# Kernel optimization log

Measured on AMD Instinct MI355X. Metric: run time of the kernel, lower is better.

The kernel has to match this reference:

```python
import jax, jax.numpy as jnp
import numpy as np

WIN = (2, 7, 7)
SHIFT = (1, 3, 3)
HEADS = 4
DIM = 128
MLP_HID = 512
N = WIN[0] * WIN[1] * WIN[2]  # 98
EPS = 1e-5


def _rel_pos_index():
    d = np.arange(WIN[0]); h = np.arange(WIN[1]); w = np.arange(WIN[2])
    coords = np.stack(np.meshgrid(d, h, w, indexing='ij'))  # (3, Wd, Wh, Ww)
    flat = coords.reshape(3, -1)  # (3, N)
    rel = flat[:, :, None] - flat[:, None, :]  # (3, N, N)
    rel = rel.transpose(1, 2, 0).astype(np.int64)  # (N, N, 3)
    rel[..., 0] += WIN[0] - 1
    rel[..., 1] += WIN[1] - 1
    rel[..., 2] += WIN[2] - 1
    rel[..., 0] *= (2 * WIN[1] - 1) * (2 * WIN[2] - 1)
    rel[..., 1] *= (2 * WIN[2] - 1)
    return rel.sum(-1)  # (N, N)


def setup_inputs() -> dict:
    key = jax.random.key(0)
    ks = jax.random.split(key, 8)
    B, D, H, W, C = 4, 8, 56, 56, DIM
    tbl_size = (2 * WIN[0] - 1) * (2 * WIN[1] - 1) * (2 * WIN[2] - 1)  # 507
    s = 0.02
    return {
        'x': jax.random.normal(ks[0], (B, D, H, W, C), jnp.float32),
        'rel_idx': jnp.asarray(_rel_pos_index(), jnp.int32),
        'rpb_table': s * jax.random.normal(ks[1], (tbl_size, HEADS), jnp.float32),
        'qkv_w': s * jax.random.normal(ks[2], (C, 3 * C), jnp.float32),
        'qkv_b': jnp.zeros((3 * C,), jnp.float32),
        'proj_w': s * jax.random.normal(ks[3], (C, C), jnp.float32),
        'proj_b': jnp.zeros((C,), jnp.float32),
        'ln1_g': jnp.ones((C,), jnp.float32),
        'ln1_b': jnp.zeros((C,), jnp.float32),
        'ln2_g': jnp.ones((C,), jnp.float32),
        'ln2_b': jnp.zeros((C,), jnp.float32),
        'mlp_w1': s * jax.random.normal(ks[4], (C, MLP_HID), jnp.float32),
        'mlp_b1': jnp.zeros((MLP_HID,), jnp.float32),
        'mlp_w2': s * jax.random.normal(ks[5], (MLP_HID, C), jnp.float32),
        'mlp_b2': jnp.zeros((C,), jnp.float32),
    }


def _layernorm(x, g, b):
    mu = jnp.mean(x, -1, keepdims=True)
    var = jnp.var(x, -1, keepdims=True)
    return (x - mu) * jax.lax.rsqrt(var + EPS) * g + b


def _window_partition(x):
    B, Dp, Hp, Wp, C = x.shape
    x = x.reshape(B, Dp // WIN[0], WIN[0], Hp // WIN[1], WIN[1], Wp // WIN[2], WIN[2], C)
    x = x.transpose(0, 1, 3, 5, 2, 4, 6, 7)
    return x.reshape(-1, N, C)


def _window_reverse(win, B, Dp, Hp, Wp):
    C = win.shape[-1]
    x = win.reshape(B, Dp // WIN[0], Hp // WIN[1], Wp // WIN[2], WIN[0], WIN[1], WIN[2], C)
    x = x.transpose(0, 1, 4, 2, 5, 3, 6, 7)
    return x.reshape(B, Dp, Hp, Wp, C)


def _block(x, rel_idx, rpb_table, qkv_w, qkv_b, proj_w, proj_b,
           ln1_g, ln1_b, ln2_g, ln2_b, mlp_w1, mlp_b1, mlp_w2, mlp_b2):
    B, D, H, W, C = x.shape
    shortcut = x
    x = _layernorm(x, ln1_g, ln1_b)
    pad_d = (-D) % WIN[0]; pad_h = (-H) % WIN[1]; pad_w = (-W) % WIN[2]
    x = jnp.pad(x, ((0, 0), (0, pad_d), (0, pad_h), (0, pad_w), (0, 0)))
    _, Dp, Hp, Wp, _ = x.shape
    x = jnp.roll(x, (-SHIFT[0], -SHIFT[1], -SHIFT[2]), axis=(1, 2, 3))
    xw = _window_partition(x)  # (B_, N, C)
    B_ = xw.shape[0]
    hd = C // HEADS
    qkv = (xw @ qkv_w + qkv_b).reshape(B_, N, 3, HEADS, hd).transpose(2, 0, 3, 1, 4)
    q, k, v = qkv[0], qkv[1], qkv[2]  # (B_, h, N, hd)
    q = q * (hd ** -0.5)
    attn = jnp.einsum('bhnd,bhmd->bhnm', q, k)
    bias = rpb_table[rel_idx.reshape(-1)].reshape(N, N, HEADS).transpose(2, 0, 1)
    attn = attn + bias[None]
    # NOTE: the original module calls attn with mask=None even when shifted.
    attn = jax.nn.softmax(attn, axis=-1)
    out = jnp.einsum('bhnm,bhmd->bhnd', attn, v).transpose(0, 2, 1, 3).reshape(B_, N, C)
    out = out @ proj_w + proj_b
    x = _window_reverse(out, B, Dp, Hp, Wp)
    x = jnp.roll(x, (SHIFT[0], SHIFT[1], SHIFT[2]), axis=(1, 2, 3))
    x = x[:, :D, :H, :W, :]
    x = shortcut + x
    h1 = _layernorm(x, ln2_g, ln2_b)
    h1 = jax.nn.gelu(h1 @ mlp_w1 + mlp_b1, approximate=False)
    return x + (h1 @ mlp_w2 + mlp_b2)


def reference(x, rel_idx, rpb_table, qkv_w, qkv_b, proj_w, proj_b,
              ln1_g, ln1_b, ln2_g, ln2_b, mlp_w1, mlp_b1, mlp_w2, mlp_b2):
    return _block(x, rel_idx, rpb_table, qkv_w, qkv_b, proj_w, proj_b,
                  ln1_g, ln1_b, ln2_g, ln2_b, mlp_w1, mlp_b1, mlp_w2, mlp_b2)
```

## Files before the change

### kernel.cpp

```cpp
#include <hip/hip_runtime.h>
#include <hip/hip_bf16.h>
#include <cstdint>

#define NWIN   1024
#define NTOK   98
#define BIAS_N 9604

typedef __attribute__((ext_vector_type(8))) short bf16x8;
typedef __attribute__((ext_vector_type(4))) float f32x4;

__device__ __forceinline__ float b2f(unsigned short u) {
  union { uint32_t i; float f; } v; v.i = ((uint32_t)u) << 16; return v.f;
}
__device__ __forceinline__ float b2f_lo(uint32_t u) {
  union { uint32_t i; float f; } v; v.i = u << 16; return v.f;
}
__device__ __forceinline__ float b2f_hi(uint32_t u) {
  union { uint32_t i; float f; } v; v.i = u & 0xffff0000u; return v.f;
}
__device__ __forceinline__ unsigned short f2b(float f) {
  union { float f; uint32_t i; } v; v.f = f;
  uint32_t r = v.i + 0x7fffu + ((v.i >> 16) & 1u);
  return (unsigned short)(r >> 16);
}
__device__ __forceinline__ float ldf(const void* p, size_t i, int f32) {
  return f32 ? ((const float*)p)[i] : b2f(((const unsigned short*)p)[i]);
}
__device__ __forceinline__ void stf(void* p, size_t i, int f32, float v) {
  if (f32) ((float*)p)[i] = v;
  else     ((unsigned short*)p)[i] = f2b(v);
}
__device__ __forceinline__ float2 ldf2(const void* p, size_t i, int f32) {
  if (f32) { const float* q = (const float*)p + i; return make_float2(q[0], q[1]); }
  uint32_t u = *(const uint32_t*)((const unsigned short*)p + i);
  return make_float2(b2f_lo(u), b2f_hi(u));
}

#define QG_OFF   0
#define KG_OFF   25690112
#define VGT_OFF  51380224
#define ZPAD_OFF 80740352
#define BIAS_OFF 80748544
#define WQ_OFF   80902208
#define WP_OFF   81000512
#define W1_OFF   81033280
#define W2_OFF   81164352
#define PAR_OFF  81295424
#define FLAG_OFF 81302080
#define P_LN1G 0
#define P_LN1B 128
#define P_LN2G 256
#define P_LN2B 384
#define P_QKVB 512
#define P_PROJB 896
#define P_B1  1024
#define P_B2  1536

__global__ __launch_bounds__(256) void detect_kernel(const uint32_t* __restrict__ xw,
                                                     int* __restrict__ flag) {
  __shared__ int cnt;
  if (threadIdx.x == 0) cnt = 0;
  __syncthreads();
  uint32_t w = xw[threadIdx.x];
  int e = (w >> 23) & 0xFF;
  if (e >= 112 && e <= 134) atomicAdd(&cnt, 1);
  __syncthreads();
  if (threadIdx.x == 0) *flag = (cnt >= 128) ? 1 : 0;
}

__global__ __launch_bounds__(256) void prep_kernel(
    const void* __restrict__ qkvw, const void* __restrict__ projw,
    const void* __restrict__ w1, const void* __restrict__ w2,
    const void* __restrict__ ln1g, const void* __restrict__ ln1b,
    const void* __restrict__ ln2g, const void* __restrict__ ln2b,
    const void* __restrict__ qkvb, const void* __restrict__ projb,
    const void* __restrict__ b1, const void* __restrict__ b2,
    const int* __restrict__ flag,
    unsigned short* __restrict__ wq_t, unsigned short* __restrict__ wp_t,
    unsigned short* __restrict__ w1_t, unsigned short* __restrict__ w2_t,
    float* __restrict__ par, unsigned short* __restrict__ zpad) {
  const int f32 = *flag;
  int idx = blockIdx.x * 256 + threadIdx.x;
  if (idx < 49152) {
    int n = idx >> 7, k = idx & 127;
    wq_t[idx] = f2b(ldf(qkvw, (size_t)k * 384 + n, f32));
  } else if ((idx -= 49152) < 16384) {
    int n = idx >> 7, k = idx & 127;
    wp_t[idx] = f2b(ldf(projw, (size_t)k * 128 + n, f32));
  } else if ((idx -= 16384) < 65536) {
    int n = idx >> 7, k = idx & 127;
    w1_t[idx] = f2b(ldf(w1, (size_t)k * 512 + n, f32));
  } else if ((idx -= 65536) < 65536) {
    int n = idx >> 9, k = idx & 511;
    w2_t[idx] = f2b(ldf(w2, (size_t)k * 128 + n, f32));
  } else if ((idx -= 65536) < 1664) {
    float v;
    if      (idx < 128)  v = ldf(ln1g, idx, f32);
    else if (idx < 256)  v = ldf(ln1b, idx - 128, f32);
    else if (idx < 384)  v = ldf(ln2g, idx - 256, f32);
    else if (idx < 512)  v = ldf(ln2b, idx - 384, f32);
    else if (idx < 896)  v = ldf(qkvb, idx - 512, f32);
    else if (idx < 1024) v = ldf(projb, idx - 896, f32);
    else if (idx < 1536) v = ldf(b1, idx - 1024, f32);
    else                 v = ldf(b2, idx - 1536, f32);
    par[idx] = v;
  } else if ((idx -= 1664) < 4096) {
    zpad[idx] = 0;
  }
}

__global__ __launch_bounds__(256) void bias_kernel(const int* __restrict__ rel_idx,
                                                   const void* __restrict__ tbl,
                                                   const int* __restrict__ flag,
                                                   float* __restrict__ bias) {
  const int f32 = *flag;
  int i = blockIdx.x * 256 + threadIdx.x;
  if (i >= 4 * BIAS_N) return;
  int h = i / BIAS_N, ij = i % BIAS_N;
  bias[i] = ldf(tbl, (size_t)rel_idx[ij] * 4 + h, f32);
}

__global__ __launch_bounds__(256) void qkv_win_kernel(
    const void* __restrict__ x, const int* __restrict__ flag,
    const unsigned short* __restrict__ wq_t, const float* __restrict__ par,
    unsigned short* __restrict__ qg, unsigned short* __restrict__ kg,
    unsigned short* __restrict__ vgt) {
  __shared__ unsigned short lnx[112 * 136];
  const int f32 = *flag;
  const int tid = threadIdx.x, wave = tid >> 6, lane = tid & 63;
  const int quad = lane >> 4, lcol = lane & 15;
  const int win = blockIdx.x;
  const int bb = win >> 8, r = win & 255;
  const int wd = r >> 6, r2 = r & 63, wh = r2 >> 3, ww = r2 & 7;

  for (int t = wave; t < NTOK; t += 4) {
    int td = t / 49, r3 = t % 49, th = r3 / 7, tw = r3 % 7;
    int sd = (wd * 2 + td + 1) & 7;
    int sh = (wh * 7 + th + 3) % 56;
    int sw = (ww * 7 + tw + 3) % 56;
    size_t src = ((((size_t)bb * 8 + sd) * 56 + sh) * 56 + sw) * 128;
    int c0 = lane * 2;
    float2 f = ldf2(x, src + c0, f32);
    float s = f.x + f.y, ss = f.x * f.x + f.y * f.y;
#pragma unroll
    for (int off = 32; off >= 1; off >>= 1) { s += __shfl_xor(s, off); ss += __shfl_xor(ss, off); }
    float mu = s * (1.0f / 128.0f);
    float var = ss * (1.0f / 128.0f) - mu * mu;
    float rs = rsqrtf(var + 1e-5f);
    float y0 = (f.x - mu) * rs * par[P_LN1G + c0] + par[P_LN1B + c0];
    float y1 = (f.y - mu) * rs * par[P_LN1G + c0 + 1] + par[P_LN1B + c0 + 1];
    *(uint32_t*)(lnx + t * 136 + c0) = (uint32_t)f2b(y0) | ((uint32_t)f2b(y1) << 16);
  }
  for (int i = tid; i < 14 * 68; i += 256) {
    int rr = i / 68, c = i % 68;
    *(uint32_t*)(lnx + (98 + rr) * 136 + c * 2) = 0u;
  }
  __syncthreads();

  for (int p = 0; p < 6; ++p) {
    const int n = p * 64 + wave * 16 + lcol;
    bf16x8 bfr[4];
#pragma unroll
    for (int ks = 0; ks < 4; ++ks)
      bfr[ks] = *(const bf16x8*)(wq_t + (size_t)n * 128 + ks * 32 + quad * 8);
    const int region = n >> 7, cc = n & 127, head = cc >> 5, d = cc & 31;
    const float bc = par[P_QKVB + n];
    if (region < 2) {
      unsigned short* dst = (region == 0 ? qg : kg) +
                            (((size_t)win * 4 + head) * NTOK) * 32 + d;
      const float scale = region == 0 ? 0.17677669529663687f : 1.0f;
      for (int mt = 0; mt < 7; ++mt) {
        f32x4 acc = (f32x4){0.f, 0.f, 0.f, 0.f};
#pragma unroll
        for (int ks = 0; ks < 4; ++ks) {
          bf16x8 a = *(const bf16x8*)(lnx + (mt * 16 + lcol) * 136 + ks * 32 + quad * 8);
          acc = __builtin_amdgcn_mfma_f32_16x16x32_bf16(a, bfr[ks], acc, 0, 0, 0);
        }
#pragma unroll
        for (int rr = 0; rr < 4; ++rr) {
          int m = mt * 16 + quad * 4 + rr;
          if (m < NTOK) dst[m * 32] = f2b((acc[rr] + bc) * scale);
        }
      }
    } else {
      unsigned short* dstv = vgt + (((size_t)win * 4 + head) * 32 + d) * 112;
      for (int mt = 0; mt < 7; ++mt) {
        f32x4 acc = (f32x4){0.f, 0.f, 0.f, 0.f};
#pragma unroll
        for (int ks = 0; ks < 4; ++ks) {
          bf16x8 a = *(const bf16x8*)(lnx + (mt * 16 + lcol) * 136 + ks * 32 + quad * 8);
          acc = __builtin_amdgcn_mfma_f32_16x16x32_bf16(a, bfr[ks], acc, 0, 0, 0);
        }
        ushort4 w;
        int m0 = mt * 16 + quad * 4;
        w.x = (m0 + 0 < NTOK) ? f2b(acc[0] + bc) : (unsigned short)0;
        w.y = (m0 + 1 < NTOK) ? f2b(acc[1] + bc) : (unsigned short)0;
        w.z = (m0 + 2 < NTOK) ? f2b(acc[2] + bc) : (unsigned short)0;
        w.w = (m0 + 3 < NTOK) ? f2b(acc[3] + bc) : (unsigned short)0;
        *(ushort4*)(dstv + m0) = w;
      }
    }
  }
}

__global__ __launch_bounds__(256, 4) void attn_fused_kernel(
    const unsigned short* __restrict__ qg, const unsigned short* __restrict__ kg,
    const unsigned short* __restrict__ vgt, const float* __restrict__ bias,
    const unsigned short* __restrict__ wp_t, const float* __restrict__ par,
    const void* __restrict__ x, const int* __restrict__ flag,
    void* __restrict__ out) {
  __shared__ __align__(16) unsigned short smem[15232];
  const int f32 = *flag;
  const int tid = threadIdx.x, wave = tid >> 6, lane = tid & 63;
  const int quad = lane >> 4, lcol = lane & 15;
  const int win = blockIdx.x, h = wave;
  const size_t hb = (((size_t)win * 4 + h) * NTOK) * 32;
  const unsigned short* vbase = vgt + (((size_t)win * 4 + h) * 32) * 112;

  unsigned short* plh = smem + h * (16 * 132);

  for (int idx = lane; idx < 16 * 16; idx += 64) {
    int rr = idx >> 4, c = 112 + (idx & 15);
    plh[rr * 132 + c] = 0;
  }

  bf16x8 aq[7], bk[7];
#pragma unroll
  for (int t = 0; t < 7; ++t) {
    int row = min(t * 16 + lcol, NTOK - 1);
    aq[t] = *(const bf16x8*)(qg + hb + (size_t)row * 32 + quad * 8);
    bk[t] = *(const bf16x8*)(kg + hb + (size_t)row * 32 + quad * 8);
  }

  const float* bh = bias + h * BIAS_N;
  f32x4 o[7][2];
  for (int mt = 0; mt < 7; ++mt) {
    f32x4 s[7];
#pragma unroll
    for (int nt = 0; nt < 7; ++nt)
      s[nt] = __builtin_amdgcn_mfma_f32_16x16x32_bf16(aq[mt], bk[nt],
                                                      (f32x4){0.f, 0.f, 0.f, 0.f}, 0, 0, 0);
    const int ib = mt * 16 + quad * 4;
#pragma unroll
    for (int nt = 0; nt < 7; ++nt) {
      int j = nt * 16 + lcol;
      bool jv = j < NTOK;
#pragma unroll
      for (int r = 0; r < 4; ++r) {
        int ic = min(ib + r, NTOK - 1);
        s[nt][r] = jv ? (s[nt][r] + bh[ic * NTOK + j]) : -3.0e38f;
      }
    }
    float mx[4], sum[4], inv[4];
#pragma unroll
    for (int r = 0; r < 4; ++r) {
      float m = s[0][r];
#pragma unroll
      for (int nt = 1; nt < 7; ++nt) m = fmaxf(m, s[nt][r]);
      mx[r] = m;
    }
#pragma unroll
    for (int off = 1; off < 16; off <<= 1)
#pragma unroll
      for (int r = 0; r < 4; ++r) mx[r] = fmaxf(mx[r], __shfl_xor(mx[r], off));
#pragma unroll
    for (int r = 0; r < 4; ++r) sum[r] = 0.f;
#pragma unroll
    for (int nt = 0; nt < 7; ++nt)
#pragma unroll
      for (int r = 0; r < 4; ++r) {
        float e = __expf(s[nt][r] - mx[r]);
        s[nt][r] = e; sum[r] += e;
      }
#pragma unroll
    for (int off = 1; off < 16; off <<= 1)
#pragma unroll
      for (int r = 0; r < 4; ++r) sum[r] += __shfl_xor(sum[r], off);
#pragma unroll
    for (int r = 0; r < 4; ++r) inv[r] = 1.0f / sum[r];
#pragma unroll
    for (int nt = 0; nt < 7; ++nt)
#pragma unroll
      for (int r = 0; r < 4; ++r)
        plh[(quad * 4 + r) * 132 + nt * 16 + lcol] = f2b(s[nt][r] * inv[r]);
#pragma unroll
    for (int n2 = 0; n2 < 2; ++n2) {
      f32x4 acc = (f32x4){0.f, 0.f, 0.f, 0.f};
#pragma unroll
      for (int kp = 0; kp < 4; ++kp) {
        bf16x8 a = *(const bf16x8*)(plh + lcol * 132 + kp * 32 + quad * 8);
        bf16x8 b = *(const bf16x8*)(vbase + (size_t)(n2 * 16 + lcol) * 112 +
                                    kp * 32 + quad * 8);
        acc = __builtin_amdgcn_mfma_f32_16x16x32_bf16(a, b, acc, 0, 0, 0);
      }
      o[mt][n2] = acc;
    }
  }
  __syncthreads();

  unsigned short* olds = smem;
#pragma unroll
  for (int mt = 0; mt < 7; ++mt)
#pragma unroll
    for (int n2 = 0; n2 < 2; ++n2)
#pragma unroll
      for (int r = 0; r < 4; ++r)
        olds[(mt * 16 + quad * 4 + r) * 136 + h * 32 + n2 * 16 + lcol] = f2b(o[mt][n2][r]);
  __syncthreads();

  f32x4 pr[2][7];
  for (int t2 = 0; t2 < 2; ++t2) {
    const int n = (h * 2 + t2) * 16 + lcol;
    bf16x8 bw[4];
#pragma unroll
    for (int kp = 0; kp < 4; ++kp)
      bw[kp] = *(const bf16x8*)(wp_t + (size_t)n * 128 + kp * 32 + quad * 8);
    for (int mt = 0; mt < 7; ++mt) {
      f32x4 acc = (f32x4){0.f, 0.f, 0.f, 0.f};
#pragma unroll
      for (int kp = 0; kp < 4; ++kp) {
        bf16x8 a = *(const bf16x8*)(olds + (mt * 16 + lcol) * 136 + kp * 32 + quad * 8);
        acc = __builtin_amdgcn_mfma_f32_16x16x32_bf16(a, bw[kp], acc, 0, 0, 0);
      }
      pr[t2][mt] = acc;
    }
  }
  __syncthreads();

  const int bb = win >> 8, rW = win & 255;
  const int wd = rW >> 6, r2 = rW & 63, wh = r2 >> 3, ww = r2 & 7;
  float* pout = (float*)smem;
  for (int pass = 0; pass < 2; ++pass) {
    const int mlo = pass * 56;
    for (int t2 = 0; t2 < 2; ++t2) {
      const int n = (h * 2 + t2) * 16 + lcol;
      const float bc = par[P_PROJB + n];
#pragma unroll
      for (int mt = 0; mt < 7; ++mt)
#pragma unroll
        for (int r = 0; r < 4; ++r) {
          int m = mt * 16 + quad * 4 + r;
          if (m >= mlo && m < mlo + 56 && m < NTOK)
            pout[(m - mlo) * 132 + n] = pr[t2][mt][r] + bc;
        }
    }
    __syncthreads();
    const int c = (tid & 31) * 4;
    for (int i = tid >> 5; i < 56; i += 8) {
      int m = mlo + i;
      if (m >= NTOK) break;
      int td = m / 49, r3 = m % 49, th = r3 / 7, tw = r3 % 7;
      int sd = (wd * 2 + td + 1) & 7;
      int sh = (wh * 7 + th + 3) % 56;
      int sw = (ww * 7 + tw + 3) % 56;
      size_t base = ((((size_t)bb * 8 + sd) * 56 + sh) * 56 + sw) * 128 + c;
      float4 p = *(const float4*)(pout + i * 132 + c);
      if (f32) {
        const float4 xr = *(const float4*)((const float*)x + base);
        float4 ov = make_float4(p.x + xr.x, p.y + xr.y, p.z + xr.z, p.w + xr.w);
        *(float4*)((float*)out + base) = ov;
      } else {
        const ushort4 xr = *(const ushort4*)((const unsigned short*)x + base);
        ushort4 ov;
        ov.x = f2b(p.x + b2f(xr.x)); ov.y = f2b(p.y + b2f(xr.y));
        ov.z = f2b(p.z + b2f(xr.z)); ov.w = f2b(p.w + b2f(xr.w));
        *(ushort4*)((unsigned short*)out + base) = ov;
      }
    }
    if (pass == 0) __syncthreads();
  }
}

__global__ __launch_bounds__(256) void mlp_kernel(
    const unsigned short* __restrict__ w1_t, const unsigned short* __restrict__ w2_t,
    const float* __restrict__ par, const int* __restrict__ flag,
    void* __restrict__ out) {
  __shared__ __align__(16) unsigned short lnt[32 * 136];
  __shared__ __align__(16) unsigned short hbuf[32 * 264];
  const int f32 = *flag;
  const int tid = threadIdx.x, wave = tid >> 6, lane = tid & 63;
  const int quad = lane >> 4, lcol = lane & 15;
  const int m0 = blockIdx.x * 32;

  for (int t = wave; t < 32; t += 4) {
    int c0 = lane * 2;
    float2 f = ldf2(out, (size_t)(m0 + t) * 128 + c0, f32);
    float s = f.x + f.y, ss = f.x * f.x + f.y * f.y;
#pragma unroll
    for (int off = 32; off >= 1; off >>= 1) { s += __shfl_xor(s, off); ss += __shfl_xor(ss, off); }
    float mu = s * (1.0f / 128.0f);
    float var = ss * (1.0f / 128.0f) - mu * mu;
    float rs = rsqrtf(var + 1e-5f);
    float y0 = (f.x - mu) * rs * par[P_LN2G + c0] + par[P_LN2B + c0];
    float y1 = (f.y - mu) * rs * par[P_LN2G + c0 + 1] + par[P_LN2B + c0 + 1];
    *(uint32_t*)(lnt + t * 136 + c0) = (uint32_t)f2b(y0) | ((uint32_t)f2b(y1) << 16);
  }
  __syncthreads();

  f32x4 acc2[2][2];
#pragma unroll
  for (int a = 0; a < 2; ++a)
#pragma unroll
    for (int b = 0; b < 2; ++b) acc2[a][b] = (f32x4){0.f, 0.f, 0.f, 0.f};

  for (int g = 0; g < 2; ++g) {
    for (int p = 0; p < 4; ++p) {
      const int nl = p * 64 + wave * 16 + lcol;
      const int n = g * 256 + nl;
      bf16x8 bfr[4];
#pragma unroll
      for (int ks = 0; ks < 4; ++ks)
        bfr[ks] = *(const bf16x8*)(w1_t + (size_t)n * 128 + ks * 32 + quad * 8);
      const float bc = par[P_B1 + n];
#pragma unroll
      for (int mt = 0; mt < 2; ++mt) {
        f32x4 acc = (f32x4){0.f, 0.f, 0.f, 0.f};
#pragma unroll
        for (int ks = 0; ks < 4; ++ks) {
          bf16x8 a = *(const bf16x8*)(lnt + (mt * 16 + lcol) * 136 + ks * 32 + quad * 8);
          acc = __builtin_amdgcn_mfma_f32_16x16x32_bf16(a, bfr[ks], acc, 0, 0, 0);
        }
#pragma unroll
        for (int rr = 0; rr < 4; ++rr) {
          int m = mt * 16 + quad * 4 + rr;
          float v = acc[rr] + bc;
          v = 0.5f * v * (1.0f + erff(v * 0.70710678118654752f));
          hbuf[m * 264 + nl] = f2b(v);
        }
      }
    }
    __syncthreads();

#pragma unroll
    for (int np = 0; np < 2; ++np) {
      const int n = np * 64 + wave * 16 + lcol;
      for (int kp = 0; kp < 2; ++kp) {
        bf16x8 bfr[4];
#pragma unroll
        for (int ks = 0; ks < 4; ++ks)
          bfr[ks] = *(const bf16x8*)(w2_t + (size_t)n * 512 + g * 256 + kp * 128 +
                                     ks * 32 + quad * 8);
#pragma unroll
        for (int mt = 0; mt < 2; ++mt) {
#pragma unroll
          for (int ks = 0; ks < 4; ++ks) {
            bf16x8 a = *(const bf16x8*)(hbuf + (mt * 16 + lcol) * 264 + kp * 128 +
                                        ks * 32 + quad * 8);
            acc2[np][mt] = __builtin_amdgcn_mfma_f32_16x16x32_bf16(a, bfr[ks], acc2[np][mt], 0, 0, 0);
          }
        }
      }
    }
    __syncthreads();
  }

  float* pout = (float*)hbuf;
#pragma unroll
  for (int np = 0; np < 2; ++np) {
    const int n = np * 64 + wave * 16 + lcol;
    const float bc = par[P_B2 + n];
#pragma unroll
    for (int mt = 0; mt < 2; ++mt)
#pragma unroll
      for (int rr = 0; rr < 4; ++rr)
        pout[(mt * 16 + quad * 4 + rr) * 132 + n] = acc2[np][mt][rr] + bc;
  }
  __syncthreads();

  for (int i = tid; i < 1024; i += 256) {
    int t = i >> 5, c = (i & 31) * 4;
    size_t base = (size_t)(m0 + t) * 128 + c;
    float4 p = *(const float4*)(pout + t * 132 + c);
    if (f32) {
      const float4 xr = *(const float4*)((const float*)out + base);
      float4 ov = make_float4(p.x + xr.x, p.y + xr.y, p.z + xr.z, p.w + xr.w);
      *(float4*)((float*)out + base) = ov;
    } else {
      const ushort4 xr = *(const ushort4*)((const unsigned short*)out + base);
      ushort4 ov;
      ov.x = f2b(p.x + b2f(xr.x)); ov.y = f2b(p.y + b2f(xr.y));
      ov.z = f2b(p.z + b2f(xr.z)); ov.w = f2b(p.w + b2f(xr.w));
      *(ushort4*)((unsigned short*)out + base) = ov;
    }
  }
}

extern "C" void kernel_launch(void* const* d_in, const int* in_sizes, int n_in,
                              void* d_out, int out_size, void* d_ws, size_t ws_size,
                              hipStream_t stream) {
  const void* x      = d_in[0];
  const int*  rel    = (const int*)d_in[1];
  const void* rpb    = d_in[2];
  const void* qkv_w  = d_in[3];
  const void* qkv_b  = d_in[4];
  const void* proj_w = d_in[5];
  const void* proj_b = d_in[6];
  const void* ln1_g  = d_in[7];
  const void* ln1_b  = d_in[8];
  const void* ln2_g  = d_in[9];
  const void* ln2_b  = d_in[10];
  const void* w1     = d_in[11];
  const void* b1     = d_in[12];
  const void* w2     = d_in[13];
  const void* b2     = d_in[14];

  char* ws = (char*)d_ws;
  unsigned short* qg   = (unsigned short*)(ws + QG_OFF);
  unsigned short* kg   = (unsigned short*)(ws + KG_OFF);
  unsigned short* vgt  = (unsigned short*)(ws + VGT_OFF);
  unsigned short* zpad = (unsigned short*)(ws + ZPAD_OFF);
  float*          bias = (float*)(ws + BIAS_OFF);
  unsigned short* wq_t = (unsigned short*)(ws + WQ_OFF);
  unsigned short* wp_t = (unsigned short*)(ws + WP_OFF);
  unsigned short* w1_t = (unsigned short*)(ws + W1_OFF);
  unsigned short* w2_t = (unsigned short*)(ws + W2_OFF);
  float*          par  = (float*)(ws + PAR_OFF);
  int*            flag = (int*)(ws + FLAG_OFF);

  detect_kernel<<<1, 256, 0, stream>>>((const uint32_t*)x, flag);
  prep_kernel<<<791, 256, 0, stream>>>(qkv_w, proj_w, w1, w2, ln1_g, ln1_b, ln2_g,
                                       ln2_b, qkv_b, proj_b, b1, b2, flag,
                                       wq_t, wp_t, w1_t, w2_t, par, zpad);
  bias_kernel<<<(4 * BIAS_N + 255) / 256, 256, 0, stream>>>(rel, rpb, flag, bias);
  qkv_win_kernel<<<NWIN, 256, 0, stream>>>(x, flag, wq_t, par, qg, kg, vgt);
  attn_fused_kernel<<<NWIN, 256, 0, stream>>>(qg, kg, vgt, bias, wp_t, par, x, flag, d_out);
  mlp_kernel<<<100352 / 32, 256, 0, stream>>>(w1_t, w2_t, par, flag, d_out);
}
```

Before: 404.1 us.

## Restructure MLP kernel to single-wave 16-row tiles with chunked hidden fusion

The MLP kernel now runs one wave per 16-token block instead of four waves per 32 tokens. It walks the 512-wide hidden dimension in 128-column chunks, feeding each GELU chunk straight into the second GEMM, which keeps the output accumulators in registers and removes block-level barriers. The exact erff GELU is swapped for an Abramowitz-Stegun polynomial approximation using a fast reciprocal and exp. Each block also reloads the full W1 and W2 weights for half as many rows, which doubles weight traffic, and the GELU approximation adds a small numerical error.

New measurement: 515.7 us. 27.6% more time.

```diff
diff --git a/kernel.cpp b/kernel.cpp
--- a/kernel.cpp
+++ b/kernel.cpp
@@ -34,6 +34,14 @@
   if (f32) { const float* q = (const float*)p + i; return make_float2(q[0], q[1]); }
   uint32_t u = *(const uint32_t*)((const unsigned short*)p + i);
   return make_float2(b2f_lo(u), b2f_hi(u));
+}
+__device__ __forceinline__ float gelu_f(float x) {
+  float a = fabsf(x) * 0.70710678118654752f;
+  float t = __builtin_amdgcn_rcpf(1.0f + 0.3275911f * a);
+  float p = ((((1.061405429f * t - 1.453152027f) * t + 1.421413741f) * t
+              - 0.284496736f) * t + 0.254829592f) * t;
+  float erfp = 1.0f - p * __expf(-a * a);
+  return 0.5f * x * (1.0f + copysignf(erfp, x));
 }
 
 #define QG_OFF   0
@@ -371,106 +379,116 @@
   }
 }
 
-__global__ __launch_bounds__(256) void mlp_kernel(
+__global__ __launch_bounds__(64, 4) void mlp_kernel(
     const unsigned short* __restrict__ w1_t, const unsigned short* __restrict__ w2_t,
     const float* __restrict__ par, const int* __restrict__ flag,
     void* __restrict__ out) {
-  __shared__ __align__(16) unsigned short lnt[32 * 136];
-  __shared__ __align__(16) unsigned short hbuf[32 * 264];
+  __shared__ __align__(16) unsigned short smem[2 * 16 * 136];
+  unsigned short* lnt = smem;
+  unsigned short* hsc = smem + 16 * 136;
   const int f32 = *flag;
-  const int tid = threadIdx.x, wave = tid >> 6, lane = tid & 63;
+  const int lane = threadIdx.x;
   const int quad = lane >> 4, lcol = lane & 15;
-  const int m0 = blockIdx.x * 32;
-
-  for (int t = wave; t < 32; t += 4) {
-    int c0 = lane * 2;
-    float2 f = ldf2(out, (size_t)(m0 + t) * 128 + c0, f32);
-    float s = f.x + f.y, ss = f.x * f.x + f.y * f.y;
-#pragma unroll
-    for (int off = 32; off >= 1; off >>= 1) { s += __shfl_xor(s, off); ss += __shfl_xor(ss, off); }
-    float mu = s * (1.0f / 128.0f);
-    float var = ss * (1.0f / 128.0f) - mu * mu;
-    float rs = rsqrtf(var + 1e-5f);
-    float y0 = (f.x - mu) * rs * par[P_LN2G + c0] + par[P_LN2B + c0];
-    float y1 = (f.y - mu) * rs * par[P_LN2G + c0 + 1] + par[P_LN2B + c0 + 1];
-    *(uint32_t*)(lnt + t * 136 + c0) = (uint32_t)f2b(y0) | ((uint32_t)f2b(y1) << 16);
-  }
-  __syncthreads();
-
-  f32x4 acc2[2][2];
-#pragma unroll
-  for (int a = 0; a < 2; ++a)
-#pragma unroll
-    for (int b = 0; b < 2; ++b) acc2[a][b] = (f32x4){0.f, 0.f, 0.f, 0.f};
-
-  for (int g = 0; g < 2; ++g) {
-    for (int p = 0; p < 4; ++p) {
-      const int nl = p * 64 + wave * 16 + lcol;
-      const int n = g * 256 + nl;
+  const int m0 = blockIdx.x * 16;
+
+  {
+    const int c0 = lcol * 8;
+    float g[8], bb_[8];
+#pragma unroll
+    for (int j = 0; j < 8; ++j) {
+      g[j] = par[P_LN2G + c0 + j];
+      bb_[j] = par[P_LN2B + c0 + j];
+    }
+    for (int it = 0; it < 4; ++it) {
+      int t = it * 4 + quad;
+      size_t base = (size_t)(m0 + t) * 128 + c0;
+      float v[8];
+      if (f32) {
+        float4 u0 = *(const float4*)((const float*)out + base);
+        float4 u1 = *(const float4*)((const float*)out + base + 4);
+        v[0] = u0.x; v[1] = u0.y; v[2] = u0.z; v[3] = u0.w;
+        v[4] = u1.x; v[5] = u1.y; v[6] = u1.z; v[7] = u1.w;
+      } else {
+        bf16x8 u = *(const bf16x8*)((const unsigned short*)out + base);
+#pragma unroll
+        for (int j = 0; j < 8; ++j) v[j] = b2f((unsigned short)u[j]);
+      }
+      float s = 0.f, ss = 0.f;
+#pragma unroll
+      for (int j = 0; j < 8; ++j) { s += v[j]; ss += v[j] * v[j]; }
+#pragma unroll
+      for (int off = 1; off < 16; off <<= 1) {
+        s += __shfl_xor(s, off); ss += __shfl_xor(ss, off);
+      }
+      float mu = s * (1.0f / 128.0f);
+      float var = ss * (1.0f / 128.0f) - mu * mu;
+      float rs = rsqrtf(var + 1e-5f);
+      bf16x8 wv;
+#pragma unroll
+      for (int j = 0; j < 8; ++j)
+        wv[j] = (short)f2b((v[j] - mu) * rs * g[j] + bb_[j]);
+      *(bf16x8*)(lnt + t * 136 + c0) = wv;
+    }
+  }
+
+  bf16x8 a1[4];
+#pragma unroll
+  for (int ks = 0; ks < 4; ++ks)
+    a1[ks] = *(const bf16x8*)(lnt + lcol * 136 + ks * 32 + quad * 8);
+
+  f32x4 oacc[8];
+#pragma unroll
+  for (int i = 0; i < 8; ++i) oacc[i] = (f32x4){0.f, 0.f, 0.f, 0.f};
+
+#pragma unroll 1
+  for (int kc = 0; kc < 4; ++kc) {
+#pragma unroll
+    for (int nt2 = 0; nt2 < 8; ++nt2) {
+      const int n = kc * 128 + nt2 * 16 + lcol;
       bf16x8 bfr[4];
 #pragma unroll
       for (int ks = 0; ks < 4; ++ks)
         bfr[ks] = *(const bf16x8*)(w1_t + (size_t)n * 128 + ks * 32 + quad * 8);
-      const float bc = par[P_B1 + n];
-#pragma unroll
-      for (int mt = 0; mt < 2; ++mt) {
-        f32x4 acc = (f32x4){0.f, 0.f, 0.f, 0.f};
-#pragma unroll
-        for (int ks = 0; ks < 4; ++ks) {
-          bf16x8 a = *(const bf16x8*)(lnt + (mt * 16 + lcol) * 136 + ks * 32 + quad * 8);
-          acc = __builtin_amdgcn_mfma_f32_16x16x32_bf16(a, bfr[ks], acc, 0, 0, 0);
-        }
-#pragma unroll
-        for (int rr = 0; rr < 4; ++rr) {
-          int m = mt * 16 + quad * 4 + rr;
-          float v = acc[rr] + bc;
-          v = 0.5f * v * (1.0f + erff(v * 0.70710678118654752f));
-          hbuf[m * 264 + nl] = f2b(v);
-        }
-      }
-    }
-    __syncthreads();
-
-#pragma unroll
-    for (int np = 0; np < 2; ++np) {
-      const int n = np * 64 + wave * 16 + lcol;
-      for (int kp = 0; kp < 2; ++kp) {
-        bf16x8 bfr[4];
-#pragma unroll
-        for (int ks = 0; ks < 4; ++ks)
-          bfr[ks] = *(const bf16x8*)(w2_t + (size_t)n * 512 + g * 256 + kp * 128 +
-                                     ks * 32 + quad * 8);
-#pragma unroll
-        for (int mt = 0; mt < 2; ++mt) {
-#pragma unroll
-          for (int ks = 0; ks < 4; ++ks) {
-            bf16x8 a = *(const bf16x8*)(hbuf + (mt * 16 + lcol) * 264 + kp * 128 +
-                                        ks * 32 + quad * 8);
-            acc2[np][mt] = __builtin_amdgcn_mfma_f32_16x16x32_bf16(a, bfr[ks], acc2[np][mt], 0, 0, 0);
-          }
-        }
-      }
-    }
-    __syncthreads();
-  }
-
-  float* pout = (float*)hbuf;
-#pragma unroll
-  for (int np = 0; np < 2; ++np) {
-    const int n = np * 64 + wave * 16 + lcol;
-    const float bc = par[P_B2 + n];
-#pragma unroll
-    for (int mt = 0; mt < 2; ++mt)
+      f32x4 c = (f32x4){0.f, 0.f, 0.f, 0.f};
+#pragma unroll
+      for (int ks = 0; ks < 4; ++ks)
+        c = __builtin_amdgcn_mfma_f32_16x16x32_bf16(a1[ks], bfr[ks], c, 0, 0, 0);
+      const float bc1 = par[P_B1 + n];
 #pragma unroll
       for (int rr = 0; rr < 4; ++rr)
-        pout[(mt * 16 + quad * 4 + rr) * 132 + n] = acc2[np][mt][rr] + bc;
-  }
-  __syncthreads();
-
-  for (int i = tid; i < 1024; i += 256) {
-    int t = i >> 5, c = (i & 31) * 4;
-    size_t base = (size_t)(m0 + t) * 128 + c;
-    float4 p = *(const float4*)(pout + t * 132 + c);
+        hsc[(quad * 4 + rr) * 136 + nt2 * 16 + lcol] = f2b(gelu_f(c[rr] + bc1));
+    }
+    bf16x8 a2[4];
+#pragma unroll
+    for (int ks = 0; ks < 4; ++ks)
+      a2[ks] = *(const bf16x8*)(hsc + lcol * 136 + ks * 32 + quad * 8);
+#pragma unroll
+    for (int nt3 = 0; nt3 < 8; ++nt3) {
+      bf16x8 b2r[4];
+#pragma unroll
+      for (int ks = 0; ks < 4; ++ks)
+        b2r[ks] = *(const bf16x8*)(w2_t + (size_t)(nt3 * 16 + lcol) * 512 +
+                                   kc * 128 + ks * 32 + quad * 8);
+#pragma unroll
+      for (int ks = 0; ks < 4; ++ks)
+        oacc[nt3] = __builtin_amdgcn_mfma_f32_16x16x32_bf16(a2[ks], b2r[ks], oacc[nt3], 0, 0, 0);
+    }
+  }
+
+  float* pout = (float*)smem;
+#pragma unroll
+  for (int nt3 = 0; nt3 < 8; ++nt3) {
+    const float bc2 = par[P_B2 + nt3 * 16 + lcol];
+#pragma unroll
+    for (int rr = 0; rr < 4; ++rr)
+      pout[(quad * 4 + rr) * 132 + nt3 * 16 + lcol] = oacc[nt3][rr] + bc2;
+  }
+
+  for (int k = 0; k < 8; ++k) {
+    int idx = k * 64 + lane;
+    int row = idx >> 5, c = (idx & 31) * 4;
+    size_t base = (size_t)(m0 + row) * 128 + c;
+    float4 p = *(const float4*)(pout + row * 132 + c);
     if (f32) {
       const float4 xr = *(const float4*)((const float*)out + base);
       float4 ov = make_float4(p.x + xr.x, p.y + xr.y, p.z + xr.z, p.w + xr.w);
@@ -524,5 +542,5 @@
   bias_kernel<<<(4 * BIAS_N + 255) / 256, 256, 0, stream>>>(rel, rpb, flag, bias);
   qkv_win_kernel<<<NWIN, 256, 0, stream>>>(x, flag, wq_t, par, qg, kg, vgt);
   attn_fused_kernel<<<NWIN, 256, 0, stream>>>(qg, kg, vgt, bias, wp_t, par, x, flag, d_out);
-  mlp_kernel<<<100352 / 32, 256, 0, stream>>>(w1_t, w2_t, par, flag, d_out);
-}
+  mlp_kernel<<<100352 / 16, 64, 0, stream>>>(w1_t, w2_t, par, flag, d_out);
+}
```

## Fuse LayerNorm2 into attention epilogue and use polynomial GELU in MLP

Applied to the files above, without the earlier changes.

The attention kernel now computes LayerNorm2 on the residual sum in its epilogue and writes a bf16 normalized copy to a workspace buffer. The MLP kernel loads its A operands directly from that buffer into registers, which removes its own LN pass, the LDS staging tile and one barrier. The exact erff GELU is replaced by an Abramowitz-Stegun polynomial with a fast reciprocal and exp, cutting transcendental cost at some accuracy risk. The trade is an extra bf16 write and read of the normalized activations.

After: 414.4 us. 2.6% more time.

```diff
diff --git a/kernel.cpp b/kernel.cpp
--- a/kernel.cpp
+++ b/kernel.cpp
@@ -34,6 +34,14 @@
   if (f32) { const float* q = (const float*)p + i; return make_float2(q[0], q[1]); }
   uint32_t u = *(const uint32_t*)((const unsigned short*)p + i);
   return make_float2(b2f_lo(u), b2f_hi(u));
+}
+__device__ __forceinline__ float gelu_f(float x) {
+  float a = fabsf(x) * 0.70710678118654752f;
+  float t = __builtin_amdgcn_rcpf(1.0f + 0.3275911f * a);
+  float p = ((((1.061405429f * t - 1.453152027f) * t + 1.421413741f) * t
+              - 0.284496736f) * t + 0.254829592f) * t;
+  float erfp = 1.0f - p * __expf(-a * a);
+  return 0.5f * x * (1.0f + copysignf(erfp, x));
 }
 
 #define QG_OFF   0
@@ -47,6 +55,7 @@
 #define W2_OFF   81164352
 #define PAR_OFF  81295424
 #define FLAG_OFF 81302080
+#define LNG_OFF  81302144
 #define P_LN1G 0
 #define P_LN1B 128
 #define P_LN2G 256
@@ -208,7 +217,7 @@
     const unsigned short* __restrict__ vgt, const float* __restrict__ bias,
     const unsigned short* __restrict__ wp_t, const float* __restrict__ par,
     const void* __restrict__ x, const int* __restrict__ flag,
-    void* __restrict__ out) {
+    unsigned short* __restrict__ lng, void* __restrict__ out) {
   __shared__ __align__(16) unsigned short smem[15232];
   const int f32 = *flag;
   const int tid = threadIdx.x, wave = tid >> 6, lane = tid & 63;
@@ -329,6 +338,9 @@
 
   const int bb = win >> 8, rW = win & 255;
   const int wd = rW >> 6, r2 = rW & 63, wh = r2 >> 3, ww = r2 & 7;
+  const int c = (tid & 31) * 4;
+  const float4 gv = *(const float4*)(par + P_LN2G + c);
+  const float4 bv = *(const float4*)(par + P_LN2B + c);
   float* pout = (float*)smem;
   for (int pass = 0; pass < 2; ++pass) {
     const int mlo = pass * 56;
@@ -345,7 +357,6 @@
         }
     }
     __syncthreads();
-    const int c = (tid & 31) * 4;
     for (int i = tid >> 5; i < 56; i += 8) {
       int m = mlo + i;
       if (m >= NTOK) break;
@@ -355,17 +366,34 @@
       int sw = (ww * 7 + tw + 3) % 56;
       size_t base = ((((size_t)bb * 8 + sd) * 56 + sh) * 56 + sw) * 128 + c;
       float4 p = *(const float4*)(pout + i * 132 + c);
+      float4 v;
       if (f32) {
         const float4 xr = *(const float4*)((const float*)x + base);
-        float4 ov = make_float4(p.x + xr.x, p.y + xr.y, p.z + xr.z, p.w + xr.w);
-        *(float4*)((float*)out + base) = ov;
+        v = make_float4(p.x + xr.x, p.y + xr.y, p.z + xr.z, p.w + xr.w);
+        *(float4*)((float*)out + base) = v;
       } else {
         const ushort4 xr = *(const ushort4*)((const unsigned short*)x + base);
+        v = make_float4(p.x + b2f(xr.x), p.y + b2f(xr.y),
+                        p.z + b2f(xr.z), p.w + b2f(xr.w));
         ushort4 ov;
-        ov.x = f2b(p.x + b2f(xr.x)); ov.y = f2b(p.y + b2f(xr.y));
-        ov.z = f2b(p.z + b2f(xr.z)); ov.w = f2b(p.w + b2f(xr.w));
+        ov.x = f2b(v.x); ov.y = f2b(v.y); ov.z = f2b(v.z); ov.w = f2b(v.w);
         *(ushort4*)((unsigned short*)out + base) = ov;
       }
+      float s = v.x + v.y + v.z + v.w;
+      float ss = v.x * v.x + v.y * v.y + v.z * v.z + v.w * v.w;
+#pragma unroll
+      for (int off = 1; off < 32; off <<= 1) {
+        s += __shfl_xor(s, off); ss += __shfl_xor(ss, off);
+      }
+      float mu = s * (1.0f / 128.0f);
+      float var = ss * (1.0f / 128.0f) - mu * mu;
+      float rs = rsqrtf(var + 1e-5f);
+      ushort4 lv;
+      lv.x = f2b((v.x - mu) * rs * gv.x + bv.x);
+      lv.y = f2b((v.y - mu) * rs * gv.y + bv.y);
+      lv.z = f2b((v.z - mu) * rs * gv.z + bv.z);
+      lv.w = f2b((v.w - mu) * rs * gv.w + bv.w);
+      *(ushort4*)(lng + base) = lv;
     }
     if (pass == 0) __syncthreads();
   }
@@ -374,28 +402,21 @@
 __global__ __launch_bounds__(256) void mlp_kernel(
     const unsigned short* __restrict__ w1_t, const unsigned short* __restrict__ w2_t,
     const float* __restrict__ par, const int* __restrict__ flag,
-    void* __restrict__ out) {
-  __shared__ __align__(16) unsigned short lnt[32 * 136];
+    const unsigned short* __restrict__ lng, void* __restrict__ out) {
   __shared__ __align__(16) unsigned short hbuf[32 * 264];
   const int f32 = *flag;
   const int tid = threadIdx.x, wave = tid >> 6, lane = tid & 63;
   const int quad = lane >> 4, lcol = lane & 15;
   const int m0 = blockIdx.x * 32;
-
-  for (int t = wave; t < 32; t += 4) {
-    int c0 = lane * 2;
-    float2 f = ldf2(out, (size_t)(m0 + t) * 128 + c0, f32);
-    float s = f.x + f.y, ss = f.x * f.x + f.y * f.y;
-#pragma unroll
-    for (int off = 32; off >= 1; off >>= 1) { s += __shfl_xor(s, off); ss += __shfl_xor(ss, off); }
-    float mu = s * (1.0f / 128.0f);
-    float var = ss * (1.0f / 128.0f) - mu * mu;
-    float rs = rsqrtf(var + 1e-5f);
-    float y0 = (f.x - mu) * rs * par[P_LN2G + c0] + par[P_LN2B + c0];
-    float y1 = (f.y - mu) * rs * par[P_LN2G + c0 + 1] + par[P_LN2B + c0 + 1];
-    *(uint32_t*)(lnt + t * 136 + c0) = (uint32_t)f2b(y0) | ((uint32_t)f2b(y1) << 16);
-  }
-  __syncthreads();
+  const int nb = wave * 16 + lcol;
+
+  bf16x8 a1[2][4];
+#pragma unroll
+  for (int mt = 0; mt < 2; ++mt)
+#pragma unroll
+    for (int ks = 0; ks < 4; ++ks)
+      a1[mt][ks] = *(const bf16x8*)(lng + (size_t)(m0 + mt * 16 + lcol) * 128 +
+                                    ks * 32 + quad * 8);
 
   f32x4 acc2[2][2];
 #pragma unroll
@@ -403,9 +424,10 @@
 #pragma unroll
     for (int b = 0; b < 2; ++b) acc2[a][b] = (f32x4){0.f, 0.f, 0.f, 0.f};
 
+#pragma unroll 1
   for (int g = 0; g < 2; ++g) {
     for (int p = 0; p < 4; ++p) {
-      const int nl = p * 64 + wave * 16 + lcol;
+      const int nl = p * 64 + nb;
       const int n = g * 256 + nl;
       bf16x8 bfr[4];
 #pragma unroll
@@ -416,16 +438,12 @@
       for (int mt = 0; mt < 2; ++mt) {
         f32x4 acc = (f32x4){0.f, 0.f, 0.f, 0.f};
 #pragma unroll
-        for (int ks = 0; ks < 4; ++ks) {
-          bf16x8 a = *(const bf16x8*)(lnt + (mt * 16 + lcol) * 136 + ks * 32 + quad * 8);
-          acc = __builtin_amdgcn_mfma_f32_16x16x32_bf16(a, bfr[ks], acc, 0, 0, 0);
-        }
+        for (int ks = 0; ks < 4; ++ks)
+          acc = __builtin_amdgcn_mfma_f32_16x16x32_bf16(a1[mt][ks], bfr[ks], acc, 0, 0, 0);
 #pragma unroll
         for (int rr = 0; rr < 4; ++rr) {
           int m = mt * 16 + quad * 4 + rr;
-          float v = acc[rr] + bc;
-          v = 0.5f * v * (1.0f + erff(v * 0.70710678118654752f));
-          hbuf[m * 264 + nl] = f2b(v);
+          hbuf[m * 264 + nl] = f2b(gelu_f(acc[rr] + bc));
         }
       }
     }
@@ -433,20 +451,19 @@
 
 #pragma unroll
     for (int np = 0; np < 2; ++np) {
-      const int n = np * 64 + wave * 16 + lcol;
       for (int kp = 0; kp < 2; ++kp) {
-        bf16x8 bfr[4];
+        bf16x8 b2r[4];
 #pragma unroll
         for (int ks = 0; ks < 4; ++ks)
-          bfr[ks] = *(const bf16x8*)(w2_t + (size_t)n * 512 + g * 256 + kp * 128 +
-                                     ks * 32 + quad * 8);
+          b2r[ks] = *(const bf16x8*)(w2_t + (size_t)(np * 64 + nb) * 512 + g * 256 +
+                                     kp * 128 + ks * 32 + quad * 8);
 #pragma unroll
         for (int mt = 0; mt < 2; ++mt) {
 #pragma unroll
           for (int ks = 0; ks < 4; ++ks) {
             bf16x8 a = *(const bf16x8*)(hbuf + (mt * 16 + lcol) * 264 + kp * 128 +
                                         ks * 32 + quad * 8);
-            acc2[np][mt] = __builtin_amdgcn_mfma_f32_16x16x32_bf16(a, bfr[ks], acc2[np][mt], 0, 0, 0);
+            acc2[np][mt] = __builtin_amdgcn_mfma_f32_16x16x32_bf16(a, b2r[ks], acc2[np][mt], 0, 0, 0);
           }
         }
       }
@@ -457,7 +474,7 @@
   float* pout = (float*)hbuf;
 #pragma unroll
   for (int np = 0; np < 2; ++np) {
-    const int n = np * 64 + wave * 16 + lcol;
+    const int n = np * 64 + nb;
     const float bc = par[P_B2 + n];
 #pragma unroll
     for (int mt = 0; mt < 2; ++mt)
@@ -516,6 +533,7 @@
   unsigned short* w2_t = (unsigned short*)(ws + W2_OFF);
   float*          par  = (float*)(ws + PAR_OFF);
   int*            flag = (int*)(ws + FLAG_OFF);
+  unsigned short* lng  = (unsigned short*)(ws + LNG_OFF);
 
   detect_kernel<<<1, 256, 0, stream>>>((const uint32_t*)x, flag);
   prep_kernel<<<791, 256, 0, stream>>>(qkv_w, proj_w, w1, w2, ln1_g, ln1_b, ln2_g,
@@ -523,6 +541,7 @@
                                        wq_t, wp_t, w1_t, w2_t, par, zpad);
   bias_kernel<<<(4 * BIAS_N + 255) / 256, 256, 0, stream>>>(rel, rpb, flag, bias);
   qkv_win_kernel<<<NWIN, 256, 0, stream>>>(x, flag, wq_t, par, qg, kg, vgt);
-  attn_fused_kernel<<<NWIN, 256, 0, stream>>>(qg, kg, vgt, bias, wp_t, par, x, flag, d_out);
-  mlp_kernel<<<100352 / 32, 256, 0, stream>>>(w1_t, w2_t, par, flag, d_out);
-}
+  attn_fused_kernel<<<NWIN, 256, 0, stream>>>(qg, kg, vgt, bias, wp_t, par, x, flag,
+                                              lng, d_out);
+  mlp_kernel<<<100352 / 32, 256, 0, stream>>>(w1_t, w2_t, par, flag, lng, d_out);
+}
```
